# Kernel tuning notes

Hardware: AMD Instinct MI355X
Metric: run time of the kernel (lower is better)

The kernel has to match this reference:

```python
import jax, jax.numpy as jnp
import numpy as np

MAXV = 8  # convex quad clipped by convex quad has at most 8 vertices


def _cr(u, v):
    return u[..., 0] * v[..., 1] - u[..., 1] * v[..., 0]


def quad_intersection_area(subj, clip):
    """Area of intersection of two convex quads via Sutherland-Hodgman.
    subj, clip: [4,2]. Replaces the pyclipper CT_INTERSECTION + Area() call."""
    # orient clip polygon CCW so the half-plane inside test (cross >= 0) is correct
    x, y = clip[:, 0], clip[:, 1]
    sa = jnp.sum(x * jnp.roll(y, -1) - jnp.roll(x, -1) * y)
    clip = jnp.where(sa < 0, clip[::-1], clip)
    edges = jnp.stack([clip, jnp.roll(clip, -1, axis=0)], axis=1)  # [4,2,2]

    pts0 = jnp.zeros((MAXV, 2), subj.dtype).at[:4].set(subj)
    n0 = jnp.int32(4)

    def clip_step(carry, edge):
        pts, n = carry
        a, b = edge[0], edge[1]
        idx = jnp.arange(MAXV)
        valid = idx < n
        nxt = jnp.where(idx + 1 >= n, 0, idx + 1)
        p, q = pts, pts[nxt]
        dp = _cr(b - a, p - a)
        dq = _cr(b - a, q - a)
        in_p, in_q = dp >= 0, dq >= 0
        denom = dp - dq
        t = jnp.where(denom == 0, 0.0, dp / jnp.where(denom == 0, 1.0, denom))
        ip = p + t[:, None] * (q - p)
        out_pts = jnp.stack([p, ip], axis=1).reshape(2 * MAXV, 2)
        out_valid = jnp.stack([valid & in_p, valid & (in_p != in_q)], axis=1).reshape(2 * MAXV)
        order = jnp.argsort(~out_valid)  # stable: valid points compacted to front
        new_pts = out_pts[order][:MAXV]
        new_n = jnp.minimum(jnp.sum(out_valid), MAXV).astype(jnp.int32)
        return (new_pts, new_n), None

    (pts, n), _ = jax.lax.scan(clip_step, (pts0, n0), edges)
    idx = jnp.arange(MAXV)
    valid = idx < n
    nxt = jnp.where(idx + 1 >= n, 0, idx + 1)
    area = 0.5 * jnp.sum(jnp.where(valid, _cr(pts, pts[nxt]), 0.0))
    return jnp.abs(area)


def _degenerate(poly):
    # original skips any quad with two identical vertices
    pairs = [(0, 1), (0, 2), (0, 3), (1, 2), (1, 3), (2, 3)]
    return jnp.any(jnp.stack([jnp.all(poly[i] == poly[j]) for i, j in pairs]))


def _per_pic(boxes, scores, polys, labels, num_class):
    P = boxes.shape[0]
    subj = boxes[:, :8].reshape(P, 4, 2)
    area_fn = jax.vmap(jax.vmap(quad_intersection_area, in_axes=(0, None)),
                       in_axes=(None, 0))
    areas = area_fn(subj, polys)                      # [G, P]
    pred_deg = jax.vmap(_degenerate)(subj)            # [P]
    gt_deg = jax.vmap(_degenerate)(polys)             # [G]
    areas = jnp.where(pred_deg[None, :], 0.0, areas)
    gmax = jnp.argmax(areas, axis=1)                  # [G]
    best = jnp.take_along_axis(areas, gmax[:, None], 1)[:, 0]
    matched = (~gt_deg) & (best != 0)
    midx = jnp.where(matched, gmax, 0)
    # unmatched rows are zeroed, exactly like pred_class_score[indices]=0
    pred_scores = jnp.where(matched[:, None], scores[midx], 0.0)
    logp = jax.nn.log_softmax(pred_scores, axis=-1)
    onehot = jax.nn.one_hot(labels, num_class, dtype=logp.dtype)
    ce = -jnp.mean(jnp.sum(onehot * logp, axis=-1))   # CrossEntropyLoss w/ soft targets
    pred_num = jnp.where(matched, jnp.argmax(scores, axis=1)[midx], -1)
    correct = jnp.sum(pred_num == labels)
    return ce, correct


def _make_quads(key, shape_prefix, img=800.0):
    k1, k2, k3 = jax.random.split(key, 3)
    c = jax.random.uniform(k1, shape_prefix + (1, 2), minval=0.0, maxval=img)
    wh = jax.random.uniform(k2, shape_prefix + (1, 2), minval=4.0, maxval=24.0)
    base = jnp.array([[-1.0, -1.0], [1.0, -1.0], [1.0, 1.0], [-1.0, 1.0]])
    jit = jax.random.uniform(k3, shape_prefix + (4, 2), minval=-1.0, maxval=1.0)
    return c + base * wh + jit


def setup_inputs() -> dict:
    key = jax.random.key(0)
    B, P, G, C = 8, 512, 128, 68
    k1, k2, k3, k4, k5 = jax.random.split(key, 5)
    pred_quads = _make_quads(k1, (B, P))              # [B,P,4,2]
    box_score = jax.random.uniform(k2, (B, P, 1))
    char_bboxes = jnp.concatenate([pred_quads.reshape(B, P, 8), box_score], axis=-1)
    char_scores = jax.random.normal(k3, (B, P, C), dtype=jnp.float32)
    polygon_chars = _make_quads(k4, (B, G))           # [B,G,4,2]
    line_chars = jax.random.randint(k5, (B, G), 0, C, dtype=jnp.int32)
    return {"char_bboxes": char_bboxes, "char_scores": char_scores,
            "polygon_chars": polygon_chars, "line_chars": line_chars}


def reference(char_bboxes, char_scores, polygon_chars, line_chars):
    C = char_scores.shape[-1]
    ce, correct = jax.vmap(lambda b, s, p, l: _per_pic(b, s, p, l, C))(
        char_bboxes, char_scores, polygon_chars, line_chars)
    loss = jnp.mean(ce)
    total_number = jnp.int32(line_chars.shape[0] * line_chars.shape[1])
    rec_correct = jnp.sum(correct).astype(jnp.int32)
    return loss, total_number, rec_correct
```

## Files before the change

kernel.cpp:

```cpp
#include <hip/hip_runtime.h>
#include <math.h>

#define B_ 8
#define P_ 512
#define G_ 128
#define C_ 68
#define BG (B_ * G_)
#define BP (B_ * P_)
#define EPS_ 1.0f

#define CLIP_EDGE(E, INX, INY, OUTX, OUTY)                                   \
    {                                                                        \
        const float eax = ccx[E], eay = ccy[E];                              \
        const float ex = ccx[(E + 1) & 3] - eax;                             \
        const float ey = ccy[(E + 1) & 3] - eay;                             \
        float vx[8], vy[8], dp[8];                                           \
        bool  vin[8];                                                        \
        _Pragma("unroll")                                                    \
        for (int i = 0; i < 8; ++i) {                                        \
            vx[i] = INX[i * 64 + lane];                                      \
            vy[i] = INY[i * 64 + lane];                                      \
        }                                                                    \
        _Pragma("unroll")                                                    \
        for (int i = 0; i < 8; ++i) {                                        \
            dp[i]  = ex * (vy[i] - eay) - ey * (vx[i] - eax);                \
            vin[i] = (dp[i] >= 0.0f);                                        \
        }                                                                    \
        int m = 0;                                                           \
        _Pragma("unroll")                                                    \
        for (int i = 0; i < 8; ++i) {                                        \
            if (i < n) {                                                     \
                const bool wrap = (i + 1 == n);                              \
                const int  jn   = (i + 1) & 7;                               \
                const float qx = wrap ? vx[0] : vx[jn];                      \
                const float qy = wrap ? vy[0] : vy[jn];                      \
                const float dq = wrap ? dp[0] : dp[jn];                      \
                const bool  inq = (dq >= 0.0f);                              \
                if (vin[i]) {                                                \
                    if (m < 8) { OUTX[m * 64 + lane] = vx[i];                \
                                 OUTY[m * 64 + lane] = vy[i]; }              \
                    ++m;                                                     \
                }                                                            \
                if (vin[i] != inq) {                                         \
                    const float den = dp[i] - dq;                            \
                    const float tt = (den == 0.0f) ? 0.0f : dp[i] / den;     \
                    if (m < 8) {                                             \
                        OUTX[m * 64 + lane] = vx[i] + tt * (qx - vx[i]);     \
                        OUTY[m * 64 + lane] = vy[i] + tt * (qy - vy[i]);     \
                    }                                                        \
                    ++m;                                                     \
                }                                                            \
            }                                                                \
        }                                                                    \
        n = (m > 8) ? 8 : m;                                                 \
    }

__global__ __launch_bounds__(256) void match_kernel(
    const float* __restrict__ bboxes,
    const float* __restrict__ scores,
    const float* __restrict__ polys,
    const int*   __restrict__ labels,
    float* __restrict__ ce_out,
    int*   __restrict__ corr_out)
{
#pragma clang fp contract(off)
    const int bg   = blockIdx.x;
    const int b    = bg >> 7;
    const int t    = threadIdx.x;
    const int w    = t >> 6;
    const int lane = t & 63;

    __shared__ int   s_seg[4 * 128];
    __shared__ int   s_cnt[4];
    __shared__ float s_px[8 * 64], s_py[8 * 64];
    __shared__ float s_qx[8 * 64], s_qy[8 * 64];

    const float* cp = polys + (size_t)bg * 8;
    const float x0 = cp[0], y0 = cp[1], x1 = cp[2], y1 = cp[3];
    const float x2 = cp[4], y2 = cp[5], x3 = cp[6], y3 = cp[7];
    const float sa = (x0 * y1 - x1 * y0) + (x1 * y2 - x2 * y1)
                   + (x2 * y3 - x3 * y2) + (x3 * y0 - x0 * y3);
    const bool rev = (sa < 0.0f);
    float ccx[4], ccy[4];
    ccx[0] = rev ? x3 : x0; ccy[0] = rev ? y3 : y0;
    ccx[1] = rev ? x2 : x1; ccy[1] = rev ? y2 : y1;
    ccx[2] = rev ? x1 : x2; ccy[2] = rev ? y1 : y2;
    ccx[3] = rev ? x0 : x3; ccy[3] = rev ? y0 : y3;
    const bool gt_deg =
        (x0 == x1 && y0 == y1) || (x0 == x2 && y0 == y2) ||
        (x0 == x3 && y0 == y3) || (x1 == x2 && y1 == y2) ||
        (x1 == x3 && y1 == y3) || (x2 == x3 && y2 == y3);
    const float glox = fminf(fminf(x0, x1), fminf(x2, x3)) - EPS_;
    const float gloy = fminf(fminf(y0, y1), fminf(y2, y3)) - EPS_;
    const float ghix = fmaxf(fmaxf(x0, x1), fmaxf(x2, x3)) + EPS_;
    const float ghiy = fmaxf(fmaxf(y0, y1), fmaxf(y2, y3)) + EPS_;

    const float* bbb = bboxes + (size_t)b * P_ * 9;
    {
        int base = 0;
        #pragma unroll
        for (int r = 0; r < 2; ++r) {
            const int p = (w << 7) + (r << 6) + lane;
            const float* bb = bbb + (size_t)p * 9;
            const float a0 = bb[0], a1 = bb[1], a2 = bb[2], a3 = bb[3];
            const float a4 = bb[4], a5 = bb[5], a6 = bb[6], a7 = bb[7];
            const bool deg =
                (a0 == a2 && a1 == a3) || (a0 == a4 && a1 == a5) ||
                (a0 == a6 && a1 == a7) || (a2 == a4 && a3 == a5) ||
                (a2 == a6 && a3 == a7) || (a4 == a6 && a5 == a7);
            const float lox = fminf(fminf(a0, a2), fminf(a4, a6));
            const float loy = fminf(fminf(a1, a3), fminf(a5, a7));
            const float hix = fmaxf(fmaxf(a0, a2), fmaxf(a4, a6));
            const float hiy = fmaxf(fmaxf(a1, a3), fmaxf(a5, a7));
            const bool ov = !deg &&
                (lox <= ghix) && (glox <= hix) &&
                (loy <= ghiy) && (gloy <= hiy);
            const unsigned long long mask = __ballot(ov);
            if (ov) {
                const int pre = __builtin_amdgcn_mbcnt_hi(
                    (unsigned int)(mask >> 32),
                    __builtin_amdgcn_mbcnt_lo((unsigned int)mask, 0u));
                s_seg[(w << 7) + base + pre] = p;
            }
            base += __popcll(mask);
        }
        if (lane == 0) s_cnt[w] = base;
    }
    __syncthreads();

    if (w != 0) return;

    const int c0 = s_cnt[0], c1 = s_cnt[1], c2 = s_cnt[2], c3 = s_cnt[3];
    const int o1 = c0, o2 = c0 + c1, o3 = c0 + c1 + c2;
    const int ns = o3 + c3;

    float bestA = 0.0f;
    int   bestI = 0x7fffffff;

    for (int k0 = 0; k0 < ns; k0 += 64) {
        const int k = k0 + lane;
        if (k < ns) {
            const int ws  = (k >= o1 ? 1 : 0) + (k >= o2 ? 1 : 0) + (k >= o3 ? 1 : 0);
            const int off = (k >= o3) ? o3 : ((k >= o2) ? o2 : ((k >= o1) ? o1 : 0));
            const int p   = s_seg[(ws << 7) + (k - off)];
            const float* bb = bbb + (size_t)p * 9;
            int n = 4;

            {
                float vx[4], vy[4], dp[4];
                bool  vin[4];
                vx[0] = bb[0]; vy[0] = bb[1];
                vx[1] = bb[2]; vy[1] = bb[3];
                vx[2] = bb[4]; vy[2] = bb[5];
                vx[3] = bb[6]; vy[3] = bb[7];
                const float eax = ccx[0], eay = ccy[0];
                const float ex = ccx[1] - eax;
                const float ey = ccy[1] - eay;
                #pragma unroll
                for (int i = 0; i < 4; ++i) {
                    dp[i]  = ex * (vy[i] - eay) - ey * (vx[i] - eax);
                    vin[i] = (dp[i] >= 0.0f);
                }
                int m = 0;
                #pragma unroll
                for (int i = 0; i < 4; ++i) {
                    const int j = (i + 1) & 3;
                    if (vin[i]) {
                        if (m < 8) { s_qx[m * 64 + lane] = vx[i];
                                     s_qy[m * 64 + lane] = vy[i]; }
                        ++m;
                    }
                    if (vin[i] != vin[j]) {
                        const float den = dp[i] - dp[j];
                        const float tt = (den == 0.0f) ? 0.0f : dp[i] / den;
                        if (m < 8) {
                            s_qx[m * 64 + lane] = vx[i] + tt * (vx[j] - vx[i]);
                            s_qy[m * 64 + lane] = vy[i] + tt * (vy[j] - vy[i]);
                        }
                        ++m;
                    }
                }
                n = (m > 8) ? 8 : m;
            }

            CLIP_EDGE(1, s_qx, s_qy, s_px, s_py)
            CLIP_EDGE(2, s_px, s_py, s_qx, s_qy)
            CLIP_EDGE(3, s_qx, s_qy, s_px, s_py)

            float s = 0.0f;
            {
                float vx[8], vy[8];
                #pragma unroll
                for (int i = 0; i < 8; ++i) {
                    vx[i] = s_px[i * 64 + lane];
                    vy[i] = s_py[i * 64 + lane];
                }
                #pragma unroll
                for (int i = 0; i < 8; ++i) {
                    if (i < n) {
                        const bool wrap = (i + 1 == n);
                        const int  jn   = (i + 1) & 7;
                        const float qx = wrap ? vx[0] : vx[jn];
                        const float qy = wrap ? vy[0] : vy[jn];
                        s += vx[i] * qy - qx * vy[i];
                    }
                }
            }
            const float area = fabsf(0.5f * s);
            if (area > bestA || (area == bestA && p < bestI)) {
                bestA = area; bestI = p;
            }
        }
    }

    #pragma unroll
    for (int off = 32; off; off >>= 1) {
        const float oa = __shfl_xor(bestA, off);
        const int   oi = __shfl_xor(bestI, off);
        if (oa > bestA || (oa == bestA && oi < bestI)) { bestA = oa; bestI = oi; }
    }

    const bool matched = (!gt_deg) && (bestA != 0.0f);
    const int label = labels[bg];

    if (matched) {
        const float* sc = scores + (size_t)(b * P_ + bestI) * C_;
        const float v0 = sc[lane];
        const bool  h2 = (lane + 64) < C_;
        const float v1 = h2 ? sc[lane + 64] : -3e38f;
        float bv; int bi;
        if (v1 > v0) { bv = v1; bi = lane + 64; } else { bv = v0; bi = lane; }
        float mx = fmaxf(v0, v1);
        #pragma unroll
        for (int off = 32; off; off >>= 1) mx = fmaxf(mx, __shfl_xor(mx, off));
        #pragma unroll
        for (int off = 32; off; off >>= 1) {
            const float ov2 = __shfl_xor(bv, off);
            const int   oi2 = __shfl_xor(bi, off);
            if (ov2 > bv || (ov2 == bv && oi2 < bi)) { bv = ov2; bi = oi2; }
        }
        float e = expf(v0 - mx) + (h2 ? expf(v1 - mx) : 0.0f);
        #pragma unroll
        for (int off = 32; off; off >>= 1) e += __shfl_xor(e, off);
        if (lane == 0) {
            ce_out[bg]   = mx + logf(e) - sc[label];
            corr_out[bg] = (bi == label) ? 1 : 0;
        }
    } else {
        if (lane == 0) {
            ce_out[bg]   = logf((float)C_);
            corr_out[bg] = 0;
        }
    }
}

__global__ __launch_bounds__(256) void finalize_kernel(
    const float* __restrict__ ce,
    const int*   __restrict__ corr,
    float* __restrict__ out)
{
    const int t = threadIdx.x;
    float a = ce[t] + ce[t + 256] + ce[t + 512] + ce[t + 768];
    int   c = corr[t] + corr[t + 256] + corr[t + 512] + corr[t + 768];
    #pragma unroll
    for (int off = 32; off; off >>= 1) {
        a += __shfl_xor(a, off);
        c += __shfl_xor(c, off);
    }
    __shared__ float pa[4];
    __shared__ int   pc[4];
    if ((t & 63) == 0) { pa[t >> 6] = a; pc[t >> 6] = c; }
    __syncthreads();
    if (t == 0) {
        const float s = (pa[0] + pa[1]) + (pa[2] + pa[3]);
        const int  cc = (pc[0] + pc[1]) + (pc[2] + pc[3]);
        out[0] = s / (float)BG;
        out[1] = (float)BG;
        out[2] = (float)cc;
    }
}

extern "C" void kernel_launch(void* const* d_in, const int* in_sizes, int n_in,
                              void* d_out, int out_size, void* d_ws, size_t ws_size,
                              hipStream_t stream) {
    const float* bboxes = (const float*)d_in[0];
    const float* scores = (const float*)d_in[1];
    const float* polys  = (const float*)d_in[2];
    const int*   labels = (const int*)d_in[3];
    float* out = (float*)d_out;

    float* ce = (float*)d_ws;
    int*   cr = (int*)((char*)d_ws + BG * sizeof(float));

    match_kernel<<<BG, 256, 0, stream>>>(bboxes, scores, polys, labels, ce, cr);
    finalize_kernel<<<1, 256, 0, stream>>>(ce, cr, out);
}
```

Before: 15.00 us.

## Fuse match and finalize kernels with last-block atomic reduction, four GTs per block

Merges the match and finalize kernels into one launch. Each 1024-thread block now handles four ground-truth polygons, and a last-block-done pattern (atomic counter plus slot array) does the final reduction. This removes a second kernel launch and the global round trip for per-GT results, and cuts the block count from 1024 to 256. In exchange, the block is larger, only 4 of its 16 waves do the clipping, and the counter relies on modulo wraparound without ever being reset.

```diff
diff --git a/kernel.cpp b/kernel.cpp
--- a/kernel.cpp
+++ b/kernel.cpp
@@ -7,6 +7,7 @@
 #define C_ 68
 #define BG (B_ * G_)
 #define BP (B_ * P_)
+#define NBLK 256
 #define EPS_ 1.0f
 
 #define CLIP_EDGE(E, INX, INY, OUTX, OUTY)                                   \
@@ -55,25 +56,34 @@
         n = (m > 8) ? 8 : m;                                                 \
     }
 
-__global__ __launch_bounds__(256) void match_kernel(
+__global__ __launch_bounds__(1024) void fused_kernel(
     const float* __restrict__ bboxes,
     const float* __restrict__ scores,
     const float* __restrict__ polys,
     const int*   __restrict__ labels,
-    float* __restrict__ ce_out,
-    int*   __restrict__ corr_out)
+    unsigned long long* __restrict__ slots,
+    unsigned int* __restrict__ counter,
+    float* __restrict__ out)
 {
 #pragma clang fp contract(off)
-    const int bg   = blockIdx.x;
-    const int b    = bg >> 7;
+    const int blk  = blockIdx.x;
     const int t    = threadIdx.x;
     const int w    = t >> 6;
     const int lane = t & 63;
-
-    __shared__ int   s_seg[4 * 128];
-    __shared__ int   s_cnt[4];
-    __shared__ float s_px[8 * 64], s_py[8 * 64];
-    __shared__ float s_qx[8 * 64], s_qy[8 * 64];
+    const int g    = w >> 2;
+    const int s    = w & 3;
+    const int bg   = (blk << 2) | g;
+    const int b    = bg >> 7;
+
+    __shared__ int   s_seg[16 * 128];
+    __shared__ int   s_cnt[16];
+    __shared__ float s_px[4 * 512], s_py[4 * 512];
+    __shared__ float s_qx[4 * 512], s_qy[4 * 512];
+    __shared__ float s_ce[4];
+    __shared__ int   s_co[4];
+    __shared__ int   s_last;
+    __shared__ float ra[4];
+    __shared__ int   rc[4];
 
     const float* cp = polys + (size_t)bg * 8;
     const float x0 = cp[0], y0 = cp[1], x1 = cp[2], y1 = cp[3];
@@ -100,7 +110,7 @@
         int base = 0;
         #pragma unroll
         for (int r = 0; r < 2; ++r) {
-            const int p = (w << 7) + (r << 6) + lane;
+            const int p = (s << 7) + (r << 6) + lane;
             const float* bb = bbb + (size_t)p * 9;
             const float a0 = bb[0], a1 = bb[1], a2 = bb[2], a3 = bb[3];
             const float a4 = bb[4], a5 = bb[5], a6 = bb[6], a7 = bb[7];
@@ -120,163 +130,179 @@
                 const int pre = __builtin_amdgcn_mbcnt_hi(
                     (unsigned int)(mask >> 32),
                     __builtin_amdgcn_mbcnt_lo((unsigned int)mask, 0u));
-                s_seg[(w << 7) + base + pre] = p;
+                s_seg[(((g << 2) | s) << 7) + base + pre] = p;
             }
             base += __popcll(mask);
         }
-        if (lane == 0) s_cnt[w] = base;
+        if (lane == 0) s_cnt[(g << 2) | s] = base;
     }
     __syncthreads();
 
-    if (w != 0) return;
-
-    const int c0 = s_cnt[0], c1 = s_cnt[1], c2 = s_cnt[2], c3 = s_cnt[3];
-    const int o1 = c0, o2 = c0 + c1, o3 = c0 + c1 + c2;
-    const int ns = o3 + c3;
-
-    float bestA = 0.0f;
-    int   bestI = 0x7fffffff;
-
-    for (int k0 = 0; k0 < ns; k0 += 64) {
-        const int k = k0 + lane;
-        if (k < ns) {
-            const int ws  = (k >= o1 ? 1 : 0) + (k >= o2 ? 1 : 0) + (k >= o3 ? 1 : 0);
-            const int off = (k >= o3) ? o3 : ((k >= o2) ? o2 : ((k >= o1) ? o1 : 0));
-            const int p   = s_seg[(ws << 7) + (k - off)];
-            const float* bb = bbb + (size_t)p * 9;
-            int n = 4;
-
-            {
-                float vx[4], vy[4], dp[4];
-                bool  vin[4];
-                vx[0] = bb[0]; vy[0] = bb[1];
-                vx[1] = bb[2]; vy[1] = bb[3];
-                vx[2] = bb[4]; vy[2] = bb[5];
-                vx[3] = bb[6]; vy[3] = bb[7];
-                const float eax = ccx[0], eay = ccy[0];
-                const float ex = ccx[1] - eax;
-                const float ey = ccy[1] - eay;
-                #pragma unroll
-                for (int i = 0; i < 4; ++i) {
-                    dp[i]  = ex * (vy[i] - eay) - ey * (vx[i] - eax);
-                    vin[i] = (dp[i] >= 0.0f);
+    if (s == 0) {
+        const int c0 = s_cnt[(g << 2) + 0], c1 = s_cnt[(g << 2) + 1];
+        const int c2 = s_cnt[(g << 2) + 2], c3 = s_cnt[(g << 2) + 3];
+        const int o1 = c0, o2 = c0 + c1, o3 = c0 + c1 + c2;
+        const int ns = o3 + c3;
+
+        float* wpx = s_px + (g << 9);
+        float* wpy = s_py + (g << 9);
+        float* wqx = s_qx + (g << 9);
+        float* wqy = s_qy + (g << 9);
+
+        float bestA = 0.0f;
+        int   bestI = 0x7fffffff;
+
+        for (int k0 = 0; k0 < ns; k0 += 64) {
+            const int k = k0 + lane;
+            if (k < ns) {
+                const int ws2 = (k >= o1 ? 1 : 0) + (k >= o2 ? 1 : 0) + (k >= o3 ? 1 : 0);
+                const int off = (k >= o3) ? o3 : ((k >= o2) ? o2 : ((k >= o1) ? o1 : 0));
+                const int p   = s_seg[(((g << 2) | ws2) << 7) + (k - off)];
+                const float* bb = bbb + (size_t)p * 9;
+                int n = 4;
+
+                {
+                    float vx[4], vy[4], dp[4];
+                    bool  vin[4];
+                    vx[0] = bb[0]; vy[0] = bb[1];
+                    vx[1] = bb[2]; vy[1] = bb[3];
+                    vx[2] = bb[4]; vy[2] = bb[5];
+                    vx[3] = bb[6]; vy[3] = bb[7];
+                    const float eax = ccx[0], eay = ccy[0];
+                    const float ex = ccx[1] - eax;
+                    const float ey = ccy[1] - eay;
+                    #pragma unroll
+                    for (int i = 0; i < 4; ++i) {
+                        dp[i]  = ex * (vy[i] - eay) - ey * (vx[i] - eax);
+                        vin[i] = (dp[i] >= 0.0f);
+                    }
+                    int m = 0;
+                    #pragma unroll
+                    for (int i = 0; i < 4; ++i) {
+                        const int j = (i + 1) & 3;
+                        if (vin[i]) {
+                            if (m < 8) { wqx[m * 64 + lane] = vx[i];
+                                         wqy[m * 64 + lane] = vy[i]; }
+                            ++m;
+                        }
+                        if (vin[i] != vin[j]) {
+                            const float den = dp[i] - dp[j];
+                            const float tt = (den == 0.0f) ? 0.0f : dp[i] / den;
+                            if (m < 8) {
+                                wqx[m * 64 + lane] = vx[i] + tt * (vx[j] - vx[i]);
+                                wqy[m * 64 + lane] = vy[i] + tt * (vy[j] - vy[i]);
+                            }
+                            ++m;
+                        }
+                    }
+                    n = (m > 8) ? 8 : m;
                 }
-                int m = 0;
-                #pragma unroll
-                for (int i = 0; i < 4; ++i) {
-                    const int j = (i + 1) & 3;
-                    if (vin[i]) {
-                        if (m < 8) { s_qx[m * 64 + lane] = vx[i];
-                                     s_qy[m * 64 + lane] = vy[i]; }
-                        ++m;
+
+                CLIP_EDGE(1, wqx, wqy, wpx, wpy)
+                CLIP_EDGE(2, wpx, wpy, wqx, wqy)
+                CLIP_EDGE(3, wqx, wqy, wpx, wpy)
+
+                float ssum = 0.0f;
+                {
+                    float vx[8], vy[8];
+                    #pragma unroll
+                    for (int i = 0; i < 8; ++i) {
+                        vx[i] = wpx[i * 64 + lane];
+                        vy[i] = wpy[i * 64 + lane];
                     }
-                    if (vin[i] != vin[j]) {
-                        const float den = dp[i] - dp[j];
-                        const float tt = (den == 0.0f) ? 0.0f : dp[i] / den;
-                        if (m < 8) {
-                            s_qx[m * 64 + lane] = vx[i] + tt * (vx[j] - vx[i]);
-                            s_qy[m * 64 + lane] = vy[i] + tt * (vy[j] - vy[i]);
+                    #pragma unroll
+                    for (int i = 0; i < 8; ++i) {
+                        if (i < n) {
+                            const bool wrap = (i + 1 == n);
+                            const int  jn   = (i + 1) & 7;
+                            const float qx = wrap ? vx[0] : vx[jn];
+                            const float qy = wrap ? vy[0] : vy[jn];
+                            ssum += vx[i] * qy - qx * vy[i];
                         }
-                        ++m;
                     }
                 }
-                n = (m > 8) ? 8 : m;
-            }
-
-            CLIP_EDGE(1, s_qx, s_qy, s_px, s_py)
-            CLIP_EDGE(2, s_px, s_py, s_qx, s_qy)
-            CLIP_EDGE(3, s_qx, s_qy, s_px, s_py)
-
-            float s = 0.0f;
-            {
-                float vx[8], vy[8];
-                #pragma unroll
-                for (int i = 0; i < 8; ++i) {
-                    vx[i] = s_px[i * 64 + lane];
-                    vy[i] = s_py[i * 64 + lane];
-                }
-                #pragma unroll
-                for (int i = 0; i < 8; ++i) {
-                    if (i < n) {
-                        const bool wrap = (i + 1 == n);
-                        const int  jn   = (i + 1) & 7;
-                        const float qx = wrap ? vx[0] : vx[jn];
-                        const float qy = wrap ? vy[0] : vy[jn];
-                        s += vx[i] * qy - qx * vy[i];
-                    }
+                const float area = fabsf(0.5f * ssum);
+                if (area > bestA || (area == bestA && p < bestI)) {
+                    bestA = area; bestI = p;
                 }
             }
-            const float area = fabsf(0.5f * s);
-            if (area > bestA || (area == bestA && p < bestI)) {
-                bestA = area; bestI = p;
-            }
-        }
-    }
-
-    #pragma unroll
-    for (int off = 32; off; off >>= 1) {
-        const float oa = __shfl_xor(bestA, off);
-        const int   oi = __shfl_xor(bestI, off);
-        if (oa > bestA || (oa == bestA && oi < bestI)) { bestA = oa; bestI = oi; }
-    }
-
-    const bool matched = (!gt_deg) && (bestA != 0.0f);
-    const int label = labels[bg];
-
-    if (matched) {
-        const float* sc = scores + (size_t)(b * P_ + bestI) * C_;
-        const float v0 = sc[lane];
-        const bool  h2 = (lane + 64) < C_;
-        const float v1 = h2 ? sc[lane + 64] : -3e38f;
-        float bv; int bi;
-        if (v1 > v0) { bv = v1; bi = lane + 64; } else { bv = v0; bi = lane; }
-        float mx = fmaxf(v0, v1);
-        #pragma unroll
-        for (int off = 32; off; off >>= 1) mx = fmaxf(mx, __shfl_xor(mx, off));
+        }
+
         #pragma unroll
         for (int off = 32; off; off >>= 1) {
-            const float ov2 = __shfl_xor(bv, off);
-            const int   oi2 = __shfl_xor(bi, off);
-            if (ov2 > bv || (ov2 == bv && oi2 < bi)) { bv = ov2; bi = oi2; }
-        }
-        float e = expf(v0 - mx) + (h2 ? expf(v1 - mx) : 0.0f);
-        #pragma unroll
-        for (int off = 32; off; off >>= 1) e += __shfl_xor(e, off);
-        if (lane == 0) {
-            ce_out[bg]   = mx + logf(e) - sc[label];
-            corr_out[bg] = (bi == label) ? 1 : 0;
-        }
-    } else {
-        if (lane == 0) {
-            ce_out[bg]   = logf((float)C_);
-            corr_out[bg] = 0;
-        }
-    }
-}
-
-__global__ __launch_bounds__(256) void finalize_kernel(
-    const float* __restrict__ ce,
-    const int*   __restrict__ corr,
-    float* __restrict__ out)
-{
-    const int t = threadIdx.x;
-    float a = ce[t] + ce[t + 256] + ce[t + 512] + ce[t + 768];
-    int   c = corr[t] + corr[t + 256] + corr[t + 512] + corr[t + 768];
-    #pragma unroll
-    for (int off = 32; off; off >>= 1) {
-        a += __shfl_xor(a, off);
-        c += __shfl_xor(c, off);
-    }
-    __shared__ float pa[4];
-    __shared__ int   pc[4];
-    if ((t & 63) == 0) { pa[t >> 6] = a; pc[t >> 6] = c; }
+            const float oa = __shfl_xor(bestA, off);
+            const int   oi = __shfl_xor(bestI, off);
+            if (oa > bestA || (oa == bestA && oi < bestI)) { bestA = oa; bestI = oi; }
+        }
+
+        const bool matched = (!gt_deg) && (bestA != 0.0f);
+        const int label = labels[bg];
+
+        float ce_val; int co_val;
+        if (matched) {
+            const float* sc = scores + (size_t)(b * P_ + bestI) * C_;
+            const float v0 = sc[lane];
+            const bool  h2 = (lane + 64) < C_;
+            const float v1 = h2 ? sc[lane + 64] : -3e38f;
+            float bv; int bi;
+            if (v1 > v0) { bv = v1; bi = lane + 64; } else { bv = v0; bi = lane; }
+            float mx = fmaxf(v0, v1);
+            #pragma unroll
+            for (int off = 32; off; off >>= 1) mx = fmaxf(mx, __shfl_xor(mx, off));
+            #pragma unroll
+            for (int off = 32; off; off >>= 1) {
+                const float ov2 = __shfl_xor(bv, off);
+                const int   oi2 = __shfl_xor(bi, off);
+                if (ov2 > bv || (ov2 == bv && oi2 < bi)) { bv = ov2; bi = oi2; }
+            }
+            float e = expf(v0 - mx) + (h2 ? expf(v1 - mx) : 0.0f);
+            #pragma unroll
+            for (int off = 32; off; off >>= 1) e += __shfl_xor(e, off);
+            ce_val = mx + logf(e) - sc[label];
+            co_val = (bi == label) ? 1 : 0;
+        } else {
+            ce_val = logf((float)C_);
+            co_val = 0;
+        }
+        if (lane == 0) { s_ce[g] = ce_val; s_co[g] = co_val; }
+    }
     __syncthreads();
+
     if (t == 0) {
-        const float s = (pa[0] + pa[1]) + (pa[2] + pa[3]);
-        const int  cc = (pc[0] + pc[1]) + (pc[2] + pc[3]);
-        out[0] = s / (float)BG;
-        out[1] = (float)BG;
-        out[2] = (float)cc;
+        const float a = ((s_ce[0] + s_ce[1]) + s_ce[2]) + s_ce[3];
+        const int   c = s_co[0] + s_co[1] + s_co[2] + s_co[3];
+        const unsigned long long pack =
+            ((unsigned long long)__float_as_uint(a) << 32) | (unsigned int)c;
+        *(volatile unsigned long long*)&slots[blk] = pack;
+        __threadfence();
+        const unsigned int tic = atomicAdd(counter, 1u);
+        s_last = ((tic & (unsigned)(NBLK - 1)) == (unsigned)(NBLK - 1)) ? 1 : 0;
+    }
+    __syncthreads();
+
+    if (s_last) {
+        __threadfence();
+        float fa = 0.0f; int fc = 0;
+        if (t < NBLK) {
+            const unsigned long long v =
+                *(volatile const unsigned long long*)&slots[t];
+            fa = __uint_as_float((unsigned int)(v >> 32));
+            fc = (int)(unsigned int)(v & 0xffffffffULL);
+            #pragma unroll
+            for (int off = 32; off; off >>= 1) {
+                fa += __shfl_xor(fa, off);
+                fc += __shfl_xor(fc, off);
+            }
+            if (lane == 0) { ra[w] = fa; rc[w] = fc; }
+        }
+        __syncthreads();
+        if (t == 0) {
+            const float stot = (ra[0] + ra[1]) + (ra[2] + ra[3]);
+            const int   ctot = rc[0] + rc[1] + rc[2] + rc[3];
+            out[0] = stot * (1.0f / (float)BG);
+            out[1] = (float)BG;
+            out[2] = (float)ctot;
+        }
     }
 }
 
@@ -289,9 +315,9 @@
     const int*   labels = (const int*)d_in[3];
     float* out = (float*)d_out;
 
-    float* ce = (float*)d_ws;
-    int*   cr = (int*)((char*)d_ws + BG * sizeof(float));
-
-    match_kernel<<<BG, 256, 0, stream>>>(bboxes, scores, polys, labels, ce, cr);
-    finalize_kernel<<<1, 256, 0, stream>>>(ce, cr, out);
+    unsigned long long* slots   = (unsigned long long*)d_ws;
+    unsigned int*       counter = (unsigned int*)((char*)d_ws + 4096);
+
+    fused_kernel<<<NBLK, 1024, 0, stream>>>(bboxes, scores, polys, labels,
+                                            slots, counter, out);
 }
```

Result: slower. 20.27 us (+35.1%).
